# Kernel tuning notes

Measured on AMD Instinct MI355X. Metric: run time of the kernel, lower is better.

## Reference

```python
import jax, jax.numpy as jnp
import numpy as np

N, E, D, G, FP = 20000, 320000, 1280, 64, 65


def _glorot(k, shape):
    s = jnp.sqrt(6.0 / (shape[0] + shape[1])).astype(jnp.float32)
    return jax.random.uniform(k, shape, jnp.float32, -s, s)


def setup_inputs() -> dict:
    key = jax.random.key(0)
    ks = jax.random.split(key, 16)
    return {
        'x': jax.random.normal(ks[0], (N, D), jnp.float32),
        'edge_index': jax.random.randint(ks[1], (2, E), 0, N),
        'batch': jnp.sort(jax.random.randint(ks[2], (N,), 0, G)),
        'fp_x': jax.random.normal(ks[3], (G, FP), jnp.float32),
        'W1': _glorot(ks[4], (D, D)), 'b1': jnp.zeros((D,), jnp.float32),
        'W2': _glorot(ks[5], (D, 640)), 'b2': jnp.zeros((640,), jnp.float32),
        'W3': _glorot(ks[6], (640, 320)), 'b3': jnp.zeros((320,), jnp.float32),
        'Wg1': _glorot(ks[7], (320, 1024)), 'bg1': jnp.zeros((1024,), jnp.float32),
        'Wg2': _glorot(ks[8], (1024, 128)), 'bg2': jnp.zeros((128,), jnp.float32),
        'Wf1': _glorot(ks[9], (193, 1024)), 'bf1': jnp.zeros((1024,), jnp.float32),
        'Wf2': _glorot(ks[10], (1024, 512)), 'bf2': jnp.zeros((512,), jnp.float32),
        'Wo': _glorot(ks[11], (512, 1)), 'bo': jnp.zeros((1,), jnp.float32),
    }


def reference(x, edge_index, batch, fp_x, W1, b1, W2, b2, W3, b3,
              Wg1, bg1, Wg2, bg2, Wf1, bf1, Wf2, bf2, Wo, bo):
    n = x.shape[0]
    g = fp_x.shape[0]
    loop = jnp.arange(n)
    src = jnp.concatenate([edge_index[0], loop])  # self-loops added (GCNConv default)
    dst = jnp.concatenate([edge_index[1], loop])
    deg = jax.ops.segment_sum(jnp.ones_like(dst, x.dtype), dst, num_segments=n)
    dis = jnp.where(deg > 0, jax.lax.rsqrt(deg), 0.0)
    norm = dis[src] * dis[dst]  # D^-1/2 (A+I) D^-1/2 edge weights

    def gcn(h, W, b):
        h = h @ W                                  # transform first (PyG GCNConv)
        agg = jax.ops.segment_sum(h[src] * norm[:, None], dst, num_segments=n)
        return agg + b

    xt = jax.nn.relu(gcn(x, W1, b1))
    xt = jax.nn.relu(gcn(xt, W2, b2))
    xt = jax.nn.relu(gcn(xt, W3, b3))
    # global mean pool over graphs
    s = jax.ops.segment_sum(xt, batch, num_segments=g)
    cnt = jax.ops.segment_sum(jnp.ones((n,), xt.dtype), batch, num_segments=g)
    xt = s / jnp.maximum(cnt, 1.0)[:, None]
    # MLP head (dropout in eval mode -> identity)
    xt = jax.nn.relu(xt @ Wg1 + bg1)
    xt = xt @ Wg2 + bg2
    xc = jnp.concatenate([fp_x, xt], axis=1)       # [G, 65+128=193]
    xc = jax.nn.relu(xc @ Wf1 + bf1)
    xc = jax.nn.relu(xc @ Wf2 + bf2)
    return xc @ Wo + bo
```

## Files before the change

### kernel.cpp

```cpp
#include <hip/hip_runtime.h>
#include <hip/hip_bf16.h>

#define N_NODES 20000
#define NPAD    20224
#define N_EDGES 320000
#define NGRAPH  64
#define FPD     65

typedef __attribute__((ext_vector_type(8))) __bf16 bf16x8;
typedef __attribute__((ext_vector_type(4))) float floatx4;
typedef __attribute__((ext_vector_type(8))) ushort ushort8v;

__device__ inline float bf2f(ushort u) {
    union { unsigned int i; float f; } c; c.i = ((unsigned int)u) << 16; return c.f;
}
__device__ inline ushort f2bf(float v) {
    __hip_bfloat16 h = __float2bfloat16(v);
    return *(ushort*)&h;
}
__device__ __forceinline__ void gld_lds16(const ushort* g, ushort* l) {
    __builtin_amdgcn_global_load_lds(
        (const __attribute__((address_space(1))) unsigned int*)g,
        (__attribute__((address_space(3))) unsigned int*)l,
        16, 0, 0);
}

__global__ void count_in(const int* __restrict__ dst, int* cnt) {
    int e = blockIdx.x * blockDim.x + threadIdx.x;
    if (e < N_EDGES) atomicAdd(&cnt[dst[e]], 1);
}
__global__ __launch_bounds__(1024) void scan_offsets(const int* __restrict__ cnt,
                                                     int* __restrict__ off, int* __restrict__ cursor,
                                                     float* __restrict__ dis) {
    __shared__ int part[1024];
    int t = threadIdx.x;
    const int chunk = (N_NODES + 1023) / 1024;
    int lo = t * chunk, hi = min(lo + chunk, N_NODES);
    int s = 0;
    for (int i = lo; i < hi; ++i) s += (cnt[i] + 4) & ~3;
    part[t] = s;
    __syncthreads();
    for (int d = 1; d < 1024; d <<= 1) {
        int v = (t >= d) ? part[t - d] : 0;
        __syncthreads();
        part[t] += v;
        __syncthreads();
    }
    int base = part[t] - s;
    for (int i = lo; i < hi; ++i) {
        int c = cnt[i] + 1;
        off[i] = base; cursor[i] = base;
        dis[i] = rsqrtf((float)c);
        base += (c + 3) & ~3;
    }
    if (t == 1023) off[N_NODES] = part[1023];
}
__global__ void fill_csr(const int* __restrict__ src, const int* __restrict__ dst,
                         const float* __restrict__ dis, int* cursor,
                         int* __restrict__ esrc, float* __restrict__ ew) {
    int e = blockIdx.x * blockDim.x + threadIdx.x;
    if (e >= N_EDGES + N_NODES) return;
    int s, d; float w;
    if (e < N_EDGES) { s = src[e]; d = dst[e]; w = dis[s] * dis[d]; }
    else { s = d = e - N_EDGES; w = dis[s] * dis[s]; }
    int pos = atomicAdd(&cursor[d], 1);
    esrc[pos] = s; ew[pos] = w;
}
__global__ void fill_pad(const int* __restrict__ off, const int* __restrict__ cursor,
                         int* __restrict__ esrc, float* __restrict__ ew) {
    int i = blockIdx.x * blockDim.x + threadIdx.x;
    if (i >= N_NODES) return;
    int e1 = off[i + 1];
    for (int e = cursor[i]; e < e1; ++e) { esrc[e] = i; ew[e] = 0.f; }
}

__global__ __launch_bounds__(256) void prep_mega(
    const float* __restrict__ x, ushort* __restrict__ xbf,
    const float* __restrict__ W1, ushort* __restrict__ Wt1,
    const float* __restrict__ W2, ushort* __restrict__ Wt2,
    const float* __restrict__ W3, ushort* __restrict__ Wt3,
    const float* __restrict__ Wf1, float* __restrict__ Wf1p,
    const float* __restrict__ fp, float* __restrict__ xc,
    const int* __restrict__ batch, int* __restrict__ gstart)
{
    __shared__ float tsh[32][33];
    int b = blockIdx.x;
    if (b < 25000) {
        int idx = b * 256 + threadIdx.x;
        int n = idx / 320, f4 = idx % 320;
        float4 v = *(const float4*)(x + (size_t)n * 1280 + f4 * 4);
        ushort4 o;
        o.x = f2bf(v.x); o.y = f2bf(v.y); o.z = f2bf(v.z); o.w = f2bf(v.w);
        *(ushort4*)(xbf + (size_t)(f4 >> 4) * (NPAD * 64) + (size_t)n * 64 + (f4 & 15) * 4) = o;
        return;
    }
    b -= 25000;
    if (b < 2600) {
        const float* W; ushort* Wt; int Nc, KP, kt, nt;
        if (b < 1600)      { W = W1; Wt = Wt1; Nc = 1280; KP = 1344; kt = b % 40; nt = b / 40; }
        else if (b < 2400) { int b2 = b - 1600; W = W2; Wt = Wt2; Nc = 640; KP = 1344; kt = b2 % 40; nt = b2 / 40; }
        else               { int b2 = b - 2400; W = W3; Wt = Wt3; Nc = 320; KP = 704;  kt = b2 % 20; nt = b2 / 20; }
        int k0 = kt * 32, n0 = nt * 32;
        int tx = threadIdx.x & 31, ty = threadIdx.x >> 5;
        #pragma unroll
        for (int i = 0; i < 4; ++i)
            tsh[ty + i * 8][tx] = W[(size_t)(k0 + ty + i * 8) * Nc + n0 + tx];
        __syncthreads();
        #pragma unroll
        for (int i = 0; i < 4; ++i)
            Wt[(size_t)(n0 + ty + i * 8) * KP + k0 + tx] = f2bf(tsh[tx][ty + i * 8]);
        return;
    }
    b -= 2600;
    if (b < 832) {
        int idx = b * 256 + threadIdx.x;
        int k = idx / 1024;
        Wf1p[idx] = (k < 193) ? Wf1[idx] : 0.f;
        return;
    }
    b -= 832;
    if (b < 52) {
        int idx = b * 256 + threadIdx.x;
        if (idx < NGRAPH * 208) {
            int g = idx / 208, j = idx % 208;
            xc[idx] = (j < FPD) ? fp[g * FPD + j] : 0.f;
        }
        return;
    }
    b -= 52;
    {
        int n = b * 256 + threadIdx.x;
        if (n >= N_NODES) return;
        int bb = batch[n];
        int bp = (n == 0) ? -1 : batch[n - 1];
        for (int g = bp + 1; g <= bb; ++g) gstart[g] = n;
        if (n == N_NODES - 1)
            for (int g = bb + 1; g <= NGRAPH; ++g) gstart[g] = N_NODES;
    }
}


#define STAGE128(AsB, BsB, kt) do {                                                   \
    const ushort* Ak_ = A + (size_t)(kt) * (NPAD * 64);                               \
    const ushort* Bk_ = Bt + (size_t)(kt) * 64;                                       \
    _Pragma("unroll")                                                                 \
    for (int i_ = 0; i_ < 4; ++i_) {                                                  \
        int c_ = tid + i_ * 256;                                                      \
        int row_ = c_ >> 3, g_ = c_ & 7;                                              \
        gld_lds16(Ak_ + (size_t)(bm + row_) * 64 + (g_ ^ (row_ & 7)) * 8, &AsB[c_ * 8]); \
    }                                                                                 \
    _Pragma("unroll")                                                                 \
    for (int i_ = 0; i_ < 4; ++i_) {                                                  \
        int c_ = tid + i_ * 256;                                                      \
        int row_ = c_ >> 3, g_ = c_ & 7;                                              \
        gld_lds16(Bk_ + (size_t)(bn + row_) * KP + (g_ ^ (row_ & 7)) * 8, &BsB[c_ * 8]); \
    }                                                                                 \
} while (0)

#define COMPUTE128(AsB, BsB) do {                                                     \
    _Pragma("unroll")                                                                 \
    for (int ks = 0; ks < 2; ++ks) {                                                  \
        bf16x8 af[4], bfv[4];                                                         \
        _Pragma("unroll")                                                             \
        for (int t = 0; t < 4; ++t) {                                                 \
            int ra = wr * 64 + t * 16 + mr;                                           \
            af[t] = *(const bf16x8*)&AsB[ra * 64 + ((ks * 4 + quad) ^ (ra & 7)) * 8]; \
            int rb = wc * 64 + t * 16 + mr;                                           \
            bfv[t] = *(const bf16x8*)&BsB[rb * 64 + ((ks * 4 + quad) ^ (rb & 7)) * 8];\
        }                                                                             \
        _Pragma("unroll")                                                             \
        for (int tm = 0; tm < 4; ++tm)                                                \
            _Pragma("unroll")                                                         \
            for (int tn = 0; tn < 4; ++tn)                                            \
                acc[tm][tn] = __builtin_amdgcn_mfma_f32_16x16x32_bf16(af[tm], bfv[tn], acc[tm][tn], 0, 0, 0); \
    }                                                                                 \
} while (0)

__global__ __launch_bounds__(256) void gemm_bf16_128(
    const ushort* __restrict__ A, const ushort* __restrict__ Bt,
    ushort* __restrict__ C, int M, int K, int KP, int Nc, int nt, int total, int chunk)
{
    __shared__ ushort As0[128 * 64], As1[128 * 64];
    __shared__ ushort Bs0[128 * 64], Bs1[128 * 64];
    const int bi = blockIdx.x;
    const int tile = (bi & 7) * chunk + (bi >> 3);
    if (tile >= total) return;
    const int bm = (tile / nt) * 128, bn = (tile % nt) * 128;

    const int tid = threadIdx.x;
    const int wid = tid >> 6, lane = tid & 63;
    const int wr = wid >> 1, wc = wid & 1;
    const int quad = lane >> 4, mr = lane & 15;

    floatx4 acc[4][4];
    #pragma unroll
    for (int i = 0; i < 4; ++i)
        #pragma unroll
        for (int j = 0; j < 4; ++j)
            acc[i][j] = (floatx4){0.f, 0.f, 0.f, 0.f};

    const int NT = K >> 6;
    STAGE128(As0, Bs0, 0);
    __syncthreads();
    for (int kt = 0; kt < NT; kt += 2) {
        if (kt + 1 < NT) STAGE128(As1, Bs1, kt + 1);
        COMPUTE128(As0, Bs0);
        __syncthreads();
        if (kt + 1 < NT) {
            if (kt + 2 < NT) STAGE128(As0, Bs0, kt + 2);
            COMPUTE128(As1, Bs1);
            __syncthreads();
        }
    }

    ushort* Cc = C + (size_t)((bn >> 6) + wc) * (NPAD * 64);
    #pragma unroll
    for (int tm = 0; tm < 4; ++tm) {
        int rowb = bm + wr * 64 + tm * 16 + quad * 4;
        #pragma unroll
        for (int r = 0; r < 4; ++r) {
            int row = rowb + r;
            if (row < M) {
                #pragma unroll
                for (int tn = 0; tn < 4; ++tn)
                    Cc[(size_t)row * 64 + tn * 16 + mr] = f2bf(acc[tm][tn][r]);
            }
        }
    }
}

#define STAGE64(AsB, BsB, kt) do {                                                    \
    const ushort* Ak_ = A + (size_t)(kt) * (NPAD * 64);                               \
    const ushort* Bk_ = Bt + (size_t)(kt) * 64;                                       \
    _Pragma("unroll")                                                                 \
    for (int i_ = 0; i_ < 8; ++i_) {                                                  \
        int c_ = tid + i_ * 256;                                                      \
        int row_ = c_ >> 3, g_ = c_ & 7;                                              \
        gld_lds16(Ak_ + (size_t)(bm + row_) * 64 + (g_ ^ (row_ & 7)) * 8, &AsB[c_ * 8]); \
    }                                                                                 \
    _Pragma("unroll")                                                                 \
    for (int i_ = 0; i_ < 2; ++i_) {                                                  \
        int c_ = tid + i_ * 256;                                                      \
        int row_ = c_ >> 3, g_ = c_ & 7;                                              \
        gld_lds16(Bk_ + (size_t)(bn + row_) * KP + (g_ ^ (row_ & 7)) * 8, &BsB[c_ * 8]); \
    }                                                                                 \
} while (0)

#define COMPUTE64(AsB, BsB) do {                                                      \
    _Pragma("unroll")                                                                 \
    for (int ks = 0; ks < 2; ++ks) {                                                  \
        bf16x8 af[4], bfv[4];                                                         \
        _Pragma("unroll")                                                             \
        for (int t = 0; t < 4; ++t) {                                                 \
            int ra = wid * 64 + t * 16 + mr;                                          \
            af[t] = *(const bf16x8*)&AsB[ra * 64 + ((ks * 4 + quad) ^ (ra & 7)) * 8]; \
            int rb = t * 16 + mr;                                                     \
            bfv[t] = *(const bf16x8*)&BsB[rb * 64 + ((ks * 4 + quad) ^ (rb & 7)) * 8];\
        }                                                                             \
        _Pragma("unroll")                                                             \
        for (int tm = 0; tm < 4; ++tm)                                                \
            _Pragma("unroll")                                                         \
            for (int tn = 0; tn < 4; ++tn)                                            \
                acc[tm][tn] = __builtin_amdgcn_mfma_f32_16x16x32_bf16(af[tm], bfv[tn], acc[tm][tn], 0, 0, 0); \
    }                                                                                 \
} while (0)

__global__ __launch_bounds__(256) void gemm_bf16(
    const ushort* __restrict__ A, const ushort* __restrict__ Bt,
    ushort* __restrict__ C, int M, int K, int KP, int Nc, int nt, int total, int chunk)
{
    __shared__ ushort As0[256 * 64], As1[256 * 64];
    __shared__ ushort Bs0[64 * 64], Bs1[64 * 64];
    const int bi = blockIdx.x;
    const int tile = (bi & 7) * chunk + (bi >> 3);
    if (tile >= total) return;
    const int bm = (tile / nt) * 256, bn = (tile % nt) * 64;

    const int tid = threadIdx.x;
    const int wid = tid >> 6, lane = tid & 63;
    const int quad = lane >> 4, mr = lane & 15;

    floatx4 acc[4][4];
    #pragma unroll
    for (int i = 0; i < 4; ++i)
        #pragma unroll
        for (int j = 0; j < 4; ++j)
            acc[i][j] = (floatx4){0.f, 0.f, 0.f, 0.f};

    const int NT = K >> 6;
    STAGE64(As0, Bs0, 0);
    __syncthreads();
    for (int kt = 0; kt < NT; kt += 2) {
        if (kt + 1 < NT) STAGE64(As1, Bs1, kt + 1);
        COMPUTE64(As0, Bs0);
        __syncthreads();
        if (kt + 1 < NT) {
            if (kt + 2 < NT) STAGE64(As0, Bs0, kt + 2);
            COMPUTE64(As1, Bs1);
            __syncthreads();
        }
    }

    ushort* Cc = C + (size_t)(bn >> 6) * (NPAD * 64);
    #pragma unroll
    for (int tm = 0; tm < 4; ++tm) {
        int rowb = bm + wid * 64 + tm * 16 + quad * 4;
        #pragma unroll
        for (int r = 0; r < 4; ++r) {
            int row = rowb + r;
            if (row < M) {
                #pragma unroll
                for (int tn = 0; tn < 4; ++tn)
                    Cc[(size_t)row * 64 + tn * 16 + mr] = f2bf(acc[tm][tn][r]);
            }
        }
    }
}

static inline void launch_gemm(const ushort* A, const ushort* Bt, ushort* C,
                               int M, int K, int KP, int Nc, hipStream_t stream) {
    if (Nc % 128 == 0) {
        int mt = (M + 127) / 128, nt = Nc / 128;
        int total = mt * nt;
        int chunk = (total + 7) / 8;
        gemm_bf16_128<<<8 * chunk, 256, 0, stream>>>(A, Bt, C, M, K, KP, Nc, nt, total, chunk);
    } else {
        int mt = (M + 255) / 256, nt = Nc / 64;
        int total = mt * nt;
        int chunk = (total + 7) / 8;
        gemm_bf16<<<8 * chunk, 256, 0, stream>>>(A, Bt, C, M, K, KP, Nc, nt, total, chunk);
    }
}

template<int TPN>
__global__ __launch_bounds__(256) void gather_tiled(
    const ushort* __restrict__ h, const int* __restrict__ off,
    const int* __restrict__ esrc, const float* __restrict__ ew,
    const float* __restrict__ bias, ushort* __restrict__ out_bf,
    float* __restrict__ out_f32, int wbf, int wf32, int nchunks, int nbpc)
{
    constexpr int NPB = 256 / TPN;
    const int bi = blockIdx.x;
    const int xcd = bi & 7;
    const int t2 = bi >> 3;
    const int s = t2 / nbpc, nb = t2 - s * nbpc;
    const int c = s * 8 + xcd;
    if (c >= nchunks) return;
    const int tid = threadIdx.x;
    const int g = tid / TPN, t = tid % TPN;
    const int n = nb * NPB + g;
    if (n >= N_NODES) return;

    const ushort* hc = h + (size_t)c * (NPAD * 64) + t * 8;
    float acc[8];
    #pragma unroll
    for (int j = 0; j < 8; ++j) acc[j] = 0.f;

    const int e0 = off[n], e1 = off[n + 1];
    for (int e = e0; e < e1; e += 4) {
        int4   s4 = *(const int4*)(esrc + e);
        float4 w4 = *(const float4*)(ew + e);
        ushort8v v0 = *(const ushort8v*)(hc + (size_t)s4.x * 64);
        ushort8v v1 = *(const ushort8v*)(hc + (size_t)s4.y * 64);
        ushort8v v2 = *(const ushort8v*)(hc + (size_t)s4.z * 64);
        ushort8v v3 = *(const ushort8v*)(hc + (size_t)s4.w * 64);
        #pragma unroll
        for (int j = 0; j < 8; ++j)
            acc[j] += w4.x * bf2f(v0[j]) + w4.y * bf2f(v1[j])
                    + w4.z * bf2f(v2[j]) + w4.w * bf2f(v3[j]);
    }

    const int fb = c * 64 + t * 8;
    float4 b0 = *(const float4*)(bias + fb);
    float4 b1 = *(const float4*)(bias + fb + 4);
    float r[8];
    r[0] = fmaxf(acc[0] + b0.x, 0.f); r[1] = fmaxf(acc[1] + b0.y, 0.f);
    r[2] = fmaxf(acc[2] + b0.z, 0.f); r[3] = fmaxf(acc[3] + b0.w, 0.f);
    r[4] = fmaxf(acc[4] + b1.x, 0.f); r[5] = fmaxf(acc[5] + b1.y, 0.f);
    r[6] = fmaxf(acc[6] + b1.z, 0.f); r[7] = fmaxf(acc[7] + b1.w, 0.f);
    if (wbf) {
        ushort8v o;
        #pragma unroll
        for (int j = 0; j < 8; ++j) o[j] = f2bf(r[j]);
        *(ushort8v*)(out_bf + (size_t)c * (NPAD * 64) + (size_t)n * 64 + t * 8) = o;
    }
    if (wf32) {
        *(float4*)(out_f32 + (size_t)n * (nchunks * 64) + fb)     = make_float4(r[0], r[1], r[2], r[3]);
        *(float4*)(out_f32 + (size_t)n * (nchunks * 64) + fb + 4) = make_float4(r[4], r[5], r[6], r[7]);
    }
}

static inline void launch_gather(const ushort* h, const int* off, const int* esrc,
                                 const float* ew, const float* bias, ushort* out_bf,
                                 float* out_f32, int wbf, int wf32, int nchunks,
                                 hipStream_t stream) {
    constexpr int TPN = 8;
    constexpr int NPB = 256 / TPN;
    const int nbpc = (N_NODES + NPB - 1) / NPB;
    const int sblocks = (nchunks + 7) / 8;
    gather_tiled<TPN><<<8 * sblocks * nbpc, 256, 0, stream>>>(
        h, off, esrc, ew, bias, out_bf, out_f32, wbf, wf32, nchunks, nbpc);
}

__global__ __launch_bounds__(320) void pool_partial(
    const float* __restrict__ x, const int* __restrict__ gstart, float* __restrict__ pool)
{
    int g = blockIdx.x, q = blockIdx.y;
    int t = threadIdx.x;
    int s = gstart[g], e = gstart[g + 1], len = e - s;
    int lo = s + (len * q) / 4, hi = s + (len * (q + 1)) / 4;
    float a0 = 0.f, a1 = 0.f, a2 = 0.f, a3 = 0.f;
    int n = lo;
    for (; n + 3 < hi; n += 4) {
        a0 += x[(size_t)(n + 0) * 320 + t];
        a1 += x[(size_t)(n + 1) * 320 + t];
        a2 += x[(size_t)(n + 2) * 320 + t];
        a3 += x[(size_t)(n + 3) * 320 + t];
    }
    for (; n < hi; ++n) a0 += x[(size_t)n * 320 + t];
    float acc = (a0 + a1) + (a2 + a3);
    if (hi > lo) atomicAdd(&pool[g * 320 + t], acc);
}

template<int K, int SPLIT, int RELU, int SCALE>
__global__ __launch_bounds__(256) void head_gemm_sk(
    const float* __restrict__ in, int istride,
    const float* __restrict__ W, const float* __restrict__ b,
    float* __restrict__ out, int M, int Nc, int ostride, int ooff,
    const int* __restrict__ gs)
{
    constexpr int KQ = K / SPLIT;
    int idx = blockIdx.x * blockDim.x + threadIdx.x;
    int oi = idx / SPLIT, r = idx % SPLIT;
    if (oi >= M * Nc) return;
    int m = oi / Nc, c = oi % Nc;
    const float* ip = in + (size_t)m * istride + r * KQ;
    const float* wp = W + (size_t)r * KQ * Nc + c;
    float a0 = 0.f, a1 = 0.f, a2 = 0.f, a3 = 0.f;
    #pragma unroll
    for (int k = 0; k < KQ; k += 4) {
        float4 v = *(const float4*)(ip + k);
        a0 += v.x * wp[(size_t)(k + 0) * Nc];
        a1 += v.y * wp[(size_t)(k + 1) * Nc];
        a2 += v.z * wp[(size_t)(k + 2) * Nc];
        a3 += v.w * wp[(size_t)(k + 3) * Nc];
    }
    float s = (a0 + a1) + (a2 + a3);
    #pragma unroll
    for (int o = 1; o < SPLIT; o <<= 1) s += __shfl_xor(s, o, 64);
    if (r == 0) {
        if (SCALE) {
            float len = (float)(gs[m + 1] - gs[m]);
            s *= 1.f / fmaxf(len, 1.f);
        }
        s += b[c];
        out[(size_t)m * ostride + ooff + c] = RELU ? fmaxf(s, 0.f) : s;
    }
}

__global__ __launch_bounds__(256) void head_out(
    const float* __restrict__ f2, const float* __restrict__ Wo,
    const float* __restrict__ bo, float* __restrict__ out)
{
    int m = blockIdx.x;
    int t = threadIdx.x;
    float2 v = *(const float2*)(f2 + (size_t)m * 512 + t * 2);
    float2 w = *(const float2*)(Wo + t * 2);
    float s = v.x * w.x + v.y * w.y;
    #pragma unroll
    for (int o = 32; o > 0; o >>= 1) s += __shfl_down(s, o, 64);
    __shared__ float ps[4];
    if ((t & 63) == 0) ps[t >> 6] = s;
    __syncthreads();
    if (t == 0) out[m] = ps[0] + ps[1] + ps[2] + ps[3] + bo[0];
}

extern "C" void kernel_launch(void* const* d_in, const int* in_sizes, int n_in,
                              void* d_out, int out_size, void* d_ws, size_t ws_size,
                              hipStream_t stream) {
    const float* x    = (const float*)d_in[0];
    const int*   eidx = (const int*)d_in[1];
    const int*   batch= (const int*)d_in[2];
    const float* fp_x = (const float*)d_in[3];
    const float* W1 = (const float*)d_in[4];  const float* b1 = (const float*)d_in[5];
    const float* W2 = (const float*)d_in[6];  const float* b2 = (const float*)d_in[7];
    const float* W3 = (const float*)d_in[8];  const float* b3 = (const float*)d_in[9];
    const float* Wg1= (const float*)d_in[10]; const float* bg1= (const float*)d_in[11];
    const float* Wg2= (const float*)d_in[12]; const float* bg2= (const float*)d_in[13];
    const float* Wf1= (const float*)d_in[14]; const float* bf1= (const float*)d_in[15];
    const float* Wf2= (const float*)d_in[16]; const float* bf2= (const float*)d_in[17];
    const float* Wo = (const float*)d_in[18]; const float* bo = (const float*)d_in[19];
    float* out = (float*)d_out;

    const int* src = eidx;
    const int* dst = eidx + N_EDGES;

    char* p = (char*)d_ws;
    float* dis   = (float*)p;  p += 20480 * 4;
    int*   cntI  = (int*)p;    p += 20480 * 4;
    int*   off   = (int*)p;    p += 20480 * 4;
    int*   cursor= (int*)p;    p += 20480 * 4;
    int*   gstart= (int*)p;    p += 128 * 4;
    int*   esrc  = (int*)p;    p += 402432 * 4;
    float* ew    = (float*)p;  p += 402432 * 4;
    ushort* xbf  = (ushort*)p; p += (size_t)NPAD * 1280 * 2;
    ushort* hbf  = (ushort*)p; p += (size_t)NPAD * 1280 * 2;
    ushort* abf  = (ushort*)p; p += (size_t)NPAD * 1280 * 2;
    float* a3f   = (float*)p;  p += (size_t)N_NODES * 320 * 4;
    ushort* Wt1  = (ushort*)p; p += (size_t)1280 * 1344 * 2;
    ushort* Wt2  = (ushort*)p; p += (size_t)640 * 1344 * 2;
    ushort* Wt3  = (ushort*)p; p += (size_t)320 * 704 * 2;
    float* pool  = (float*)p;  p += NGRAPH * 320 * 4;
    float* m1    = (float*)p;  p += NGRAPH * 1024 * 4;
    float* xc    = (float*)p;  p += NGRAPH * 208 * 4;
    float* f1    = (float*)p;  p += NGRAPH * 1024 * 4;
    float* f2    = (float*)p;  p += NGRAPH * 512 * 4;
    float* Wf1p  = (float*)p;  p += 208 * 1024 * 4;

    hipMemsetAsync(cntI, 0, N_NODES * 4, stream);
    hipMemsetAsync(pool, 0, NGRAPH * 320 * 4, stream);

    prep_mega<<<25000 + 2600 + 832 + 52 + 79, 256, 0, stream>>>(
        x, xbf, W1, Wt1, W2, Wt2, W3, Wt3, Wf1, Wf1p, fp_x, xc, batch, gstart);

    count_in<<<(N_EDGES + 255) / 256, 256, 0, stream>>>(dst, cntI);
    scan_offsets<<<1, 1024, 0, stream>>>(cntI, off, cursor, dis);
    fill_csr<<<(N_EDGES + N_NODES + 255) / 256, 256, 0, stream>>>(src, dst, dis, cursor, esrc, ew);
    fill_pad<<<(N_NODES + 255) / 256, 256, 0, stream>>>(off, cursor, esrc, ew);

    launch_gemm(xbf, Wt1, hbf, N_NODES, 1280, 1344, 1280, stream);
    launch_gather(hbf, off, esrc, ew, b1, abf, (float*)nullptr, 1, 0, 20, stream);
    launch_gemm(abf, Wt2, hbf, N_NODES, 1280, 1344, 640, stream);
    launch_gather(hbf, off, esrc, ew, b2, abf, (float*)nullptr, 1, 0, 10, stream);
    launch_gemm(abf, Wt3, hbf, N_NODES, 640, 704, 320, stream);
    launch_gather(hbf, off, esrc, ew, b3, (ushort*)nullptr, a3f, 0, 1, 5, stream);

    pool_partial<<<dim3(NGRAPH, 4), 320, 0, stream>>>(a3f, gstart, pool);

    head_gemm_sk<320, 4, 1, 1><<<(NGRAPH * 1024 * 4 + 255) / 256, 256, 0, stream>>>(
        pool, 320, Wg1, bg1, m1, NGRAPH, 1024, 1024, 0, gstart);
    head_gemm_sk<1024, 8, 0, 0><<<(NGRAPH * 128 * 8 + 255) / 256, 256, 0, stream>>>(
        m1, 1024, Wg2, bg2, xc, NGRAPH, 128, 208, FPD, (const int*)nullptr);
    head_gemm_sk<208, 4, 1, 0><<<(NGRAPH * 1024 * 4 + 255) / 256, 256, 0, stream>>>(
        xc, 208, Wf1p, bf1, f1, NGRAPH, 1024, 1024, 0, (const int*)nullptr);
    head_gemm_sk<1024, 8, 1, 0><<<(NGRAPH * 512 * 8 + 255) / 256, 256, 0, stream>>>(
        f1, 1024, Wf2, bf2, f2, NGRAPH, 512, 512, 0, (const int*)nullptr);
    head_out<<<NGRAPH, 256, 0, stream>>>(f2, Wo, bo, out);
}
```

Baseline: 698.7 us.

## Bucket nodes by padded degree to balance gather warps, remap block-to-XCD assignment

Adds a single-block kernel that counting-sorts nodes by padded in-degree bucket into a permutation, and the gather kernel now processes nodes in that order. Nodes with similar edge counts share a wavefront, which is meant to cut divergence from uneven loop trip counts. The block index mapping also changes so each XCD gets a contiguous range of (chunk, node-block) work instead of interleaved chunks. The cost is one extra serial launch, an indirect node lookup, and output writes that are scattered rather than sequential.

```diff
diff --git a/kernel.cpp b/kernel.cpp
--- a/kernel.cpp
+++ b/kernel.cpp
@@ -54,6 +54,29 @@
         base += (c + 3) & ~3;
     }
     if (t == 1023) off[N_NODES] = part[1023];
+}
+__global__ __launch_bounds__(1024) void build_perm(const int* __restrict__ cnt,
+                                                   int* __restrict__ perm) {
+    __shared__ int hist[64];
+    __shared__ int base[64];
+    int t = threadIdx.x;
+    if (t < 64) hist[t] = 0;
+    __syncthreads();
+    for (int i = t; i < N_NODES; i += 1024) {
+        int g = ((cnt[i] + 4) & ~3) >> 2;
+        atomicAdd(&hist[min(g, 63)], 1);
+    }
+    __syncthreads();
+    if (t == 0) {
+        int acc = 0;
+        for (int b = 0; b < 64; ++b) { base[b] = acc; acc += hist[b]; }
+    }
+    __syncthreads();
+    for (int i = t; i < N_NODES; i += 1024) {
+        int g = ((cnt[i] + 4) & ~3) >> 2;
+        int pos = atomicAdd(&base[min(g, 63)], 1);
+        perm[pos] = i;
+    }
 }
 __global__ void fill_csr(const int* __restrict__ src, const int* __restrict__ dst,
                          const float* __restrict__ dis, int* cursor,
@@ -337,19 +360,19 @@
     const ushort* __restrict__ h, const int* __restrict__ off,
     const int* __restrict__ esrc, const float* __restrict__ ew,
     const float* __restrict__ bias, ushort* __restrict__ out_bf,
-    float* __restrict__ out_f32, int wbf, int wf32, int nchunks, int nbpc)
+    float* __restrict__ out_f32, const int* __restrict__ perm,
+    int wbf, int wf32, int nchunks, int nbpc, int cpx)
 {
     constexpr int NPB = 256 / TPN;
     const int bi = blockIdx.x;
-    const int xcd = bi & 7;
-    const int t2 = bi >> 3;
-    const int s = t2 / nbpc, nb = t2 - s * nbpc;
-    const int c = s * 8 + xcd;
-    if (c >= nchunks) return;
+    const int t2 = (bi & 7) * cpx + (bi >> 3);
+    if (t2 >= nchunks * nbpc) return;
+    const int c = t2 / nbpc, nb = t2 - c * nbpc;
     const int tid = threadIdx.x;
     const int g = tid / TPN, t = tid % TPN;
-    const int n = nb * NPB + g;
-    if (n >= N_NODES) return;
+    const int np = nb * NPB + g;
+    if (np >= N_NODES) return;
+    const int n = perm[np];
 
     const ushort* hc = h + (size_t)c * (NPAD * 64) + t * 8;
     float acc[8];
@@ -392,14 +415,15 @@
 
 static inline void launch_gather(const ushort* h, const int* off, const int* esrc,
                                  const float* ew, const float* bias, ushort* out_bf,
-                                 float* out_f32, int wbf, int wf32, int nchunks,
-                                 hipStream_t stream) {
+                                 float* out_f32, const int* perm,
+                                 int wbf, int wf32, int nchunks, hipStream_t stream) {
     constexpr int TPN = 8;
     constexpr int NPB = 256 / TPN;
     const int nbpc = (N_NODES + NPB - 1) / NPB;
-    const int sblocks = (nchunks + 7) / 8;
-    gather_tiled<TPN><<<8 * sblocks * nbpc, 256, 0, stream>>>(
-        h, off, esrc, ew, bias, out_bf, out_f32, wbf, wf32, nchunks, nbpc);
+    const int total = nchunks * nbpc;
+    const int cpx = (total + 7) / 8;
+    gather_tiled<TPN><<<8 * cpx, 256, 0, stream>>>(
+        h, off, esrc, ew, bias, out_bf, out_f32, perm, wbf, wf32, nchunks, nbpc, cpx);
 }
 
 __global__ __launch_bounds__(320) void pool_partial(
@@ -500,6 +524,7 @@
     int*   cntI  = (int*)p;    p += 20480 * 4;
     int*   off   = (int*)p;    p += 20480 * 4;
     int*   cursor= (int*)p;    p += 20480 * 4;
+    int*   perm  = (int*)p;    p += 20480 * 4;
     int*   gstart= (int*)p;    p += 128 * 4;
     int*   esrc  = (int*)p;    p += 402432 * 4;
     float* ew    = (float*)p;  p += 402432 * 4;
@@ -524,16 +549,17 @@
         x, xbf, W1, Wt1, W2, Wt2, W3, Wt3, Wf1, Wf1p, fp_x, xc, batch, gstart);
 
     count_in<<<(N_EDGES + 255) / 256, 256, 0, stream>>>(dst, cntI);
+    build_perm<<<1, 1024, 0, stream>>>(cntI, perm);
     scan_offsets<<<1, 1024, 0, stream>>>(cntI, off, cursor, dis);
     fill_csr<<<(N_EDGES + N_NODES + 255) / 256, 256, 0, stream>>>(src, dst, dis, cursor, esrc, ew);
     fill_pad<<<(N_NODES + 255) / 256, 256, 0, stream>>>(off, cursor, esrc, ew);
 
     launch_gemm(xbf, Wt1, hbf, N_NODES, 1280, 1344, 1280, stream);
-    launch_gather(hbf, off, esrc, ew, b1, abf, (float*)nullptr, 1, 0, 20, stream);
+    launch_gather(hbf, off, esrc, ew, b1, abf, (float*)nullptr, perm, 1, 0, 20, stream);
     launch_gemm(abf, Wt2, hbf, N_NODES, 1280, 1344, 640, stream);
-    launch_gather(hbf, off, esrc, ew, b2, abf, (float*)nullptr, 1, 0, 10, stream);
+    launch_gather(hbf, off, esrc, ew, b2, abf, (float*)nullptr, perm, 1, 0, 10, stream);
     launch_gemm(abf, Wt3, hbf, N_NODES, 640, 704, 320, stream);
-    launch_gather(hbf, off, esrc, ew, b3, (ushort*)nullptr, a3f, 0, 1, 5, stream);
+    launch_gather(hbf, off, esrc, ew, b3, (ushort*)nullptr, a3f, perm, 0, 1, 5, stream);
 
     pool_partial<<<dim3(NGRAPH, 4), 320, 0, stream>>>(a3f, gstart, pool);
 
```

Measured after the change: 660.1 us. 5.5% less time.
